# Kernel optimization log

Hardware: AMD Instinct MI355X
Metric: run time of the kernel (lower is better)

## Reference

```python
import jax, jax.numpy as jnp
import numpy as np

BATCH = 512          # bs_large + bs_small
COMBINED_BS = 320    # bs_large + bs_small // (r_large // r_small)
R = 64               # r_large
K = 4096             # hidden dim, fixed in the TIR kernel
N_ADAPT = 80         # combined adapters


def setup_inputs() -> dict:
    key = jax.random.key(0)
    k1, k2, k3, k4 = jax.random.split(key, 4)
    x = jax.random.normal(k1, (BATCH, 1, K), dtype=jnp.float32)
    xids = jax.random.randint(k2, (COMBINED_BS * R,), 0, BATCH, dtype=jnp.int32)
    wids = jax.random.randint(k3, (COMBINED_BS,), 0, N_ADAPT, dtype=jnp.int32)
    A = jax.random.normal(k4, (N_ADAPT, K, R), dtype=jnp.float32) * 0.02
    return {"x": x, "xids": xids, "wids": wids, "A": A}


def reference(x, xids, wids, A):
    # out[c, 0, r] = sum_k x[xids[c*R + r], 0, k] * A[wids[c], k, r]
    C = wids.shape[0]
    r = A.shape[2]
    tok = xids.reshape(C, r)          # per-output-element token ids
    xg = x[tok, 0, :]                 # (C, R, K) gathered activations
    Ag = A[wids]                      # (C, K, R) gathered adapters
    out = jnp.einsum('crk,ckr->cr', xg, Ag)
    return out[:, None, :]            # (C, 1, R)
```

## Files before the change

kernel.cpp:

```cpp
#include <hip/hip_runtime.h>
#include <stdint.h>

namespace {
constexpr int BATCH  = 512;
constexpr int CBS    = 320;
constexpr int R      = 64;
constexpr int K      = 4096;
constexpr int NADAPT = 80;
constexpr int SPLIT  = 8;
constexpr int KS     = K / SPLIT;
constexpr int TK     = 64;
constexpr int NT     = 256;
constexpr int NW     = NT / 64;
constexpr int NTILES = KS / TK;

constexpr size_t WS_X_OFF  = 4096;
constexpr size_t WS_NEEDED = WS_X_OFF + (size_t)BATCH * K * 2;

__device__ inline uint16_t f2bf(float f) {
    uint32_t u = __float_as_uint(f);
    u += 0x7fffu + ((u >> 16) & 1u);
    return (uint16_t)(u >> 16);
}
__device__ inline float bf2f(uint16_t b) {
    return __uint_as_float((uint32_t)b << 16);
}
__device__ inline float bflo(uint32_t u) { return __uint_as_float(u << 16); }
__device__ inline float bfhi(uint32_t u) { return __uint_as_float(u & 0xffff0000u); }
}

__global__ __launch_bounds__(256)
void prep(const float* __restrict__ x, uint16_t* __restrict__ xb,
          const int* __restrict__ wids, int* __restrict__ perm,
          float* __restrict__ out, int out_size)
{
    const int bid = blockIdx.x;
    const int t   = threadIdx.x;
    if (bid == 0) {
        __shared__ int hist[NADAPT];
        __shared__ int offs[NADAPT];
        if (t < NADAPT) hist[t] = 0;
        __syncthreads();
        for (int c = t; c < CBS; c += 256) atomicAdd(&hist[wids[c]], 1);
        __syncthreads();
        if (t == 0) {
            int run = 0;
            for (int i = 0; i < NADAPT; ++i) { offs[i] = run; run += hist[i]; }
        }
        __syncthreads();
        for (int c = t; c < CBS; c += 256) {
            const int pos = atomicAdd(&offs[wids[c]], 1);
            perm[pos] = c;
        }
    } else if (bid <= BATCH * K / 1024) {
        const int i = (bid - 1) * 256 + t;
        const float4 v = ((const float4*)x)[i];
        ushort4 o;
        o.x = f2bf(v.x); o.y = f2bf(v.y); o.z = f2bf(v.z); o.w = f2bf(v.w);
        ((ushort4*)xb)[i] = o;
    } else {
        const int i4 = (bid - (1 + BATCH * K / 1024)) * 256 + t;
        const int e  = i4 * 4;
        if (e + 3 < out_size) {
            ((float4*)out)[i4] = make_float4(0.f, 0.f, 0.f, 0.f);
        } else {
            for (int q = e; q < out_size; ++q) out[q] = 0.f;
        }
    }
}

__global__ __launch_bounds__(NT, 8)
void lora_main(const int* __restrict__ xids,
               const int* __restrict__ wids,
               const float* __restrict__ A,
               const uint16_t* __restrict__ xb,
               const int* __restrict__ perm,
               float* __restrict__ out)
{
    __shared__ uint32_t xs[2][(TK / 2) * R];
    __shared__ float red[NW * R];

    const int bid  = blockIdx.x;
    const int i0   = bid >> 3;
    const int s    = bid & 7;
    const int c    = perm[i0];
    const int t    = threadIdx.x;
    const int wv   = t >> 6;
    const int lane = t & 63;
    const int r4   = lane & 15;
    const int kq   = lane >> 4;

    const int wid = wids[c];
    const float* __restrict__ Aw = A + (size_t)wid * (K * R);

    const int kc = t & 15;
    const int rg = t >> 4;
    uint32_t rowoff[4];
#pragma unroll
    for (int j = 0; j < 4; ++j)
        rowoff[j] = (uint32_t)xids[c * R + 4 * rg + j] * K;
    const uint16_t* __restrict__ xbase = xb + (size_t)s * KS + kc * 4;
    const int colw = (4 * rg) ^ (kc << 2);
    const int w0i  = (2 * kc + 0) * R + colw;
    const int w1i  = (2 * kc + 1) * R + colw;

    const size_t aBase = (size_t)(s * KS + 16 * wv + 2 * kq) * R + 4 * r4;

    float4 acc = make_float4(0.f, 0.f, 0.f, 0.f);

    {
        uint2 L0 = *(const uint2*)(xbase + rowoff[0]);
        uint2 L1 = *(const uint2*)(xbase + rowoff[1]);
        uint2 L2 = *(const uint2*)(xbase + rowoff[2]);
        uint2 L3 = *(const uint2*)(xbase + rowoff[3]);
        *(uint4*)&xs[0][w0i] = make_uint4(L0.x, L1.x, L2.x, L3.x);
        *(uint4*)&xs[0][w1i] = make_uint4(L0.y, L1.y, L2.y, L3.y);
    }

    uint2 P0, P1, P2, P3;
    for (int tile = 0; tile < NTILES; ++tile) {
        const int nt = tile + 1;
        if (nt < NTILES) {
            const uint16_t* src = xbase + nt * TK;
            P0 = *(const uint2*)(src + rowoff[0]);
            P1 = *(const uint2*)(src + rowoff[1]);
            P2 = *(const uint2*)(src + rowoff[2]);
            P3 = *(const uint2*)(src + rowoff[3]);
        }
        __syncthreads();

        {
            const uint32_t* __restrict__ B = xs[tile & 1];
            const float* __restrict__ At = Aw + aBase + (size_t)tile * TK * R;
#pragma unroll
            for (int i = 0; i < 2; ++i) {
                const int k2  = wv * 8 + kq + 4 * i;
                const int col = (4 * r4) ^ (((k2 >> 1) & 15) << 2);
                const uint4 xv = *(const uint4*)&B[k2 * R + col];
                const float* Ap = At + (size_t)(8 * i) * R;
                const float4 a0 = *(const float4*)Ap;
                const float4 a1 = *(const float4*)(Ap + R);
                acc.x = fmaf(bflo(xv.x), a0.x, acc.x);
                acc.x = fmaf(bfhi(xv.x), a1.x, acc.x);
                acc.y = fmaf(bflo(xv.y), a0.y, acc.y);
                acc.y = fmaf(bfhi(xv.y), a1.y, acc.y);
                acc.z = fmaf(bflo(xv.z), a0.z, acc.z);
                acc.z = fmaf(bfhi(xv.z), a1.z, acc.z);
                acc.w = fmaf(bflo(xv.w), a0.w, acc.w);
                acc.w = fmaf(bfhi(xv.w), a1.w, acc.w);
            }
        }

        if (nt < NTILES) {
            const int b = nt & 1;
            *(uint4*)&xs[b][w0i] = make_uint4(P0.x, P1.x, P2.x, P3.x);
            *(uint4*)&xs[b][w1i] = make_uint4(P0.y, P1.y, P2.y, P3.y);
        }
    }

#pragma unroll
    for (int m = 16; m < 64; m <<= 1) {
        acc.x += __shfl_xor(acc.x, m, 64);
        acc.y += __shfl_xor(acc.y, m, 64);
        acc.z += __shfl_xor(acc.z, m, 64);
        acc.w += __shfl_xor(acc.w, m, 64);
    }
    __syncthreads();
    if (kq == 0) {
        float* rd = &red[wv * R + 4 * r4];
        rd[0] = acc.x; rd[1] = acc.y; rd[2] = acc.z; rd[3] = acc.w;
    }
    __syncthreads();
    if (wv == 0) {
        float sum = red[lane] + red[R + lane] + red[2 * R + lane] + red[3 * R + lane];
        atomicAdd(&out[c * R + lane], sum);
    }
}

__global__ __launch_bounds__(NT)
void lora_fallback(const float* __restrict__ x,
                   const int*   __restrict__ xids,
                   const int*   __restrict__ wids,
                   const float* __restrict__ A,
                   float*       __restrict__ out)
{
    __shared__ float xsf[TK * R];
    __shared__ float red[NW * R];
    const int bid  = blockIdx.x;
    const int c    = bid >> 3;
    const int s    = bid & 7;
    const int t    = threadIdx.x;
    const int wave = t >> 6;
    const int lane = t & 63;
    const int r4   = lane & 15;
    const int kq   = lane >> 4;
    const int wid  = wids[c];
    const float* __restrict__ Aw = A + (size_t)wid * (K * R);
    const int rw  = t >> 2;
    const int jq  = t & 3;
    const int tok = xids[c * R + rw];
    const float* __restrict__ xrow = x + (size_t)tok * K + s * KS + jq * 16;
    float4 acc = make_float4(0.f, 0.f, 0.f, 0.f);
    float4 pv[4];
    {
        const float4* src = (const float4*)xrow;
#pragma unroll
        for (int ii = 0; ii < 4; ++ii) pv[ii] = src[ii];
    }
    for (int tile = 0; tile < NTILES; ++tile) {
#pragma unroll
        for (int ii = 0; ii < 4; ++ii) {
            const int kk = jq * 16 + ii * 4;
            xsf[(kk + 0) * R + rw] = pv[ii].x;
            xsf[(kk + 1) * R + rw] = pv[ii].y;
            xsf[(kk + 2) * R + rw] = pv[ii].z;
            xsf[(kk + 3) * R + rw] = pv[ii].w;
        }
        __syncthreads();
        if (tile + 1 < NTILES) {
            const float4* src = (const float4*)(xrow + (tile + 1) * TK);
#pragma unroll
            for (int ii = 0; ii < 4; ++ii) pv[ii] = src[ii];
        }
        const int kw = wave * 16 + kq;
        const float* __restrict__ Ap =
            Aw + (size_t)(s * KS + tile * TK + kw) * R + 4 * r4;
#pragma unroll
        for (int i = 0; i < 4; ++i) {
            float4 av = *(const float4*)(Ap + (size_t)(4 * i) * R);
            float4 xv = *(const float4*)(&xsf[(kw + 4 * i) * R + 4 * r4]);
            acc.x = fmaf(xv.x, av.x, acc.x);
            acc.y = fmaf(xv.y, av.y, acc.y);
            acc.z = fmaf(xv.z, av.z, acc.z);
            acc.w = fmaf(xv.w, av.w, acc.w);
        }
        __syncthreads();
    }
#pragma unroll
    for (int m = 16; m < 64; m <<= 1) {
        acc.x += __shfl_xor(acc.x, m, 64);
        acc.y += __shfl_xor(acc.y, m, 64);
        acc.z += __shfl_xor(acc.z, m, 64);
        acc.w += __shfl_xor(acc.w, m, 64);
    }
    if (kq == 0) {
        float* rd = &red[wave * R + 4 * r4];
        rd[0] = acc.x; rd[1] = acc.y; rd[2] = acc.z; rd[3] = acc.w;
    }
    __syncthreads();
    if (wave == 0) {
        float sum = red[lane] + red[R + lane] + red[2 * R + lane] + red[3 * R + lane];
        atomicAdd(&out[c * R + lane], sum);
    }
}

extern "C" void kernel_launch(void* const* d_in, const int* in_sizes, int n_in,
                              void* d_out, int out_size, void* d_ws, size_t ws_size,
                              hipStream_t stream)
{
    (void)in_sizes; (void)n_in;
    const float* x    = (const float*)d_in[0];
    const int*   xids = (const int*)d_in[1];
    const int*   wids = (const int*)d_in[2];
    const float* A    = (const float*)d_in[3];
    float* out        = (float*)d_out;

    if (ws_size >= WS_NEEDED) {
        int*      perm = (int*)d_ws;
        uint16_t* xbw  = (uint16_t*)((char*)d_ws + WS_X_OFF);
        const int ncvt = BATCH * K / 1024;
        const int nz   = (out_size + 1023) / 1024;
        hipLaunchKernelGGL(prep, dim3(1 + ncvt + nz), dim3(256), 0, stream,
                           x, xbw, wids, perm, out, out_size);
        hipLaunchKernelGGL(lora_main, dim3(CBS * SPLIT), dim3(NT), 0, stream,
                           xids, wids, A, xbw, perm, out);
    } else {
        hipMemsetAsync(out, 0, (size_t)out_size * sizeof(float), stream);
        hipLaunchKernelGGL(lora_fallback, dim3(CBS * SPLIT), dim3(NT), 0, stream,
                           x, xids, wids, A, out);
    }
}
```

Baseline: 149.2 us.

## Process four combined rows per block with direct register loads, sharing A when adapters match

The main kernel is restructured. Each block now handles a group of four perm-sorted combined rows over one of 16 K-splits. Each thread owns one output column r and streams its gathered bf16 x row directly with 16-byte loads, dropping the LDS transpose, the double buffering and the block reductions. When the group's first and last rows share an adapter (sorted by perm), A values are loaded once and reused across all four rows, cutting A traffic. The trade-off is uncoalesced-looking per-thread x row loads (each lane reads a different token row) and more atomics per output.

```diff
diff --git a/kernel.cpp b/kernel.cpp
--- a/kernel.cpp
+++ b/kernel.cpp
@@ -7,12 +7,12 @@
 constexpr int R      = 64;
 constexpr int K      = 4096;
 constexpr int NADAPT = 80;
-constexpr int SPLIT  = 8;
+constexpr int GRP    = 4;
+constexpr int NGRP   = CBS / GRP;
+constexpr int SPLIT  = 16;
 constexpr int KS     = K / SPLIT;
-constexpr int TK     = 64;
+constexpr int KW     = KS / 4;
 constexpr int NT     = 256;
-constexpr int NW     = NT / 64;
-constexpr int NTILES = KS / TK;
 
 constexpr size_t WS_X_OFF  = 4096;
 constexpr size_t WS_NEEDED = WS_X_OFF + (size_t)BATCH * K * 2;
@@ -21,9 +21,6 @@
     uint32_t u = __float_as_uint(f);
     u += 0x7fffu + ((u >> 16) & 1u);
     return (uint16_t)(u >> 16);
-}
-__device__ inline float bf2f(uint16_t b) {
-    return __uint_as_float((uint32_t)b << 16);
 }
 __device__ inline float bflo(uint32_t u) { return __uint_as_float(u << 16); }
 __device__ inline float bfhi(uint32_t u) { return __uint_as_float(u & 0xffff0000u); }
@@ -69,7 +66,7 @@
     }
 }
 
-__global__ __launch_bounds__(NT, 8)
+__global__ __launch_bounds__(NT)
 void lora_main(const int* __restrict__ xids,
                const int* __restrict__ wids,
                const float* __restrict__ A,
@@ -77,104 +74,82 @@
                const int* __restrict__ perm,
                float* __restrict__ out)
 {
-    __shared__ uint32_t xs[2][(TK / 2) * R];
-    __shared__ float red[NW * R];
-
-    const int bid  = blockIdx.x;
-    const int i0   = bid >> 3;
-    const int s    = bid & 7;
-    const int c    = perm[i0];
-    const int t    = threadIdx.x;
-    const int wv   = t >> 6;
-    const int lane = t & 63;
-    const int r4   = lane & 15;
-    const int kq   = lane >> 4;
-
-    const int wid = wids[c];
-    const float* __restrict__ Aw = A + (size_t)wid * (K * R);
-
-    const int kc = t & 15;
-    const int rg = t >> 4;
-    uint32_t rowoff[4];
-#pragma unroll
-    for (int j = 0; j < 4; ++j)
-        rowoff[j] = (uint32_t)xids[c * R + 4 * rg + j] * K;
-    const uint16_t* __restrict__ xbase = xb + (size_t)s * KS + kc * 4;
-    const int colw = (4 * rg) ^ (kc << 2);
-    const int w0i  = (2 * kc + 0) * R + colw;
-    const int w1i  = (2 * kc + 1) * R + colw;
-
-    const size_t aBase = (size_t)(s * KS + 16 * wv + 2 * kq) * R + 4 * r4;
-
-    float4 acc = make_float4(0.f, 0.f, 0.f, 0.f);
-
-    {
-        uint2 L0 = *(const uint2*)(xbase + rowoff[0]);
-        uint2 L1 = *(const uint2*)(xbase + rowoff[1]);
-        uint2 L2 = *(const uint2*)(xbase + rowoff[2]);
-        uint2 L3 = *(const uint2*)(xbase + rowoff[3]);
-        *(uint4*)&xs[0][w0i] = make_uint4(L0.x, L1.x, L2.x, L3.x);
-        *(uint4*)&xs[0][w1i] = make_uint4(L0.y, L1.y, L2.y, L3.y);
-    }
-
-    uint2 P0, P1, P2, P3;
-    for (int tile = 0; tile < NTILES; ++tile) {
-        const int nt = tile + 1;
-        if (nt < NTILES) {
-            const uint16_t* src = xbase + nt * TK;
-            P0 = *(const uint2*)(src + rowoff[0]);
-            P1 = *(const uint2*)(src + rowoff[1]);
-            P2 = *(const uint2*)(src + rowoff[2]);
-            P3 = *(const uint2*)(src + rowoff[3]);
-        }
-        __syncthreads();
-
-        {
-            const uint32_t* __restrict__ B = xs[tile & 1];
-            const float* __restrict__ At = Aw + aBase + (size_t)tile * TK * R;
-#pragma unroll
-            for (int i = 0; i < 2; ++i) {
-                const int k2  = wv * 8 + kq + 4 * i;
-                const int col = (4 * r4) ^ (((k2 >> 1) & 15) << 2);
-                const uint4 xv = *(const uint4*)&B[k2 * R + col];
-                const float* Ap = At + (size_t)(8 * i) * R;
-                const float4 a0 = *(const float4*)Ap;
-                const float4 a1 = *(const float4*)(Ap + R);
-                acc.x = fmaf(bflo(xv.x), a0.x, acc.x);
-                acc.x = fmaf(bfhi(xv.x), a1.x, acc.x);
-                acc.y = fmaf(bflo(xv.y), a0.y, acc.y);
-                acc.y = fmaf(bfhi(xv.y), a1.y, acc.y);
-                acc.z = fmaf(bflo(xv.z), a0.z, acc.z);
-                acc.z = fmaf(bfhi(xv.z), a1.z, acc.z);
-                acc.w = fmaf(bflo(xv.w), a0.w, acc.w);
-                acc.w = fmaf(bfhi(xv.w), a1.w, acc.w);
+    const int bid = blockIdx.x;
+    const int g   = bid >> 4;
+    const int s   = bid & 15;
+    const int t   = threadIdx.x;
+    const int wv  = t >> 6;
+    const int r   = t & 63;
+    const int k0  = s * KS + wv * KW;
+
+    const int c0 = perm[GRP * g + 0], c1 = perm[GRP * g + 1],
+              c2 = perm[GRP * g + 2], c3 = perm[GRP * g + 3];
+    const int w0 = wids[c0], w1 = wids[c1], w2 = wids[c2], w3 = wids[c3];
+
+    const uint16_t* __restrict__ xp0 = xb + (size_t)xids[c0 * R + r] * K + k0;
+    const uint16_t* __restrict__ xp1 = xb + (size_t)xids[c1 * R + r] * K + k0;
+    const uint16_t* __restrict__ xp2 = xb + (size_t)xids[c2 * R + r] * K + k0;
+    const uint16_t* __restrict__ xp3 = xb + (size_t)xids[c3 * R + r] * K + k0;
+
+    const size_t kb = (size_t)k0 * R + r;
+    const float* __restrict__ A0 = A + (size_t)w0 * (K * R) + kb;
+    const float* __restrict__ A1 = A + (size_t)w1 * (K * R) + kb;
+    const float* __restrict__ A2 = A + (size_t)w2 * (K * R) + kb;
+    const float* __restrict__ A3 = A + (size_t)w3 * (K * R) + kb;
+
+    float acc0 = 0.f, acc1 = 0.f, acc2 = 0.f, acc3 = 0.f;
+
+#define FMA8(ACC, V, AP) do {                                              \
+        ACC = fmaf(bflo((V).x), (AP)[0], ACC);                             \
+        ACC = fmaf(bfhi((V).x), (AP)[1], ACC);                             \
+        ACC = fmaf(bflo((V).y), (AP)[2], ACC);                             \
+        ACC = fmaf(bfhi((V).y), (AP)[3], ACC);                             \
+        ACC = fmaf(bflo((V).z), (AP)[4], ACC);                             \
+        ACC = fmaf(bfhi((V).z), (AP)[5], ACC);                             \
+        ACC = fmaf(bflo((V).w), (AP)[6], ACC);                             \
+        ACC = fmaf(bfhi((V).w), (AP)[7], ACC);                             \
+    } while (0)
+
+    if (w0 == w3) {
+#pragma unroll 2
+        for (int kk = 0; kk < KW; kk += 8) {
+            const uint4 v0 = *(const uint4*)(xp0 + kk);
+            const uint4 v1 = *(const uint4*)(xp1 + kk);
+            const uint4 v2 = *(const uint4*)(xp2 + kk);
+            const uint4 v3 = *(const uint4*)(xp3 + kk);
+            float a[8];
+#pragma unroll
+            for (int q = 0; q < 8; ++q) a[q] = A0[(size_t)(kk + q) * R];
+            FMA8(acc0, v0, a);
+            FMA8(acc1, v1, a);
+            FMA8(acc2, v2, a);
+            FMA8(acc3, v3, a);
+        }
+    } else {
+#pragma unroll 2
+        for (int kk = 0; kk < KW; kk += 8) {
+            const uint4 v0 = *(const uint4*)(xp0 + kk);
+            const uint4 v1 = *(const uint4*)(xp1 + kk);
+            const uint4 v2 = *(const uint4*)(xp2 + kk);
+            const uint4 v3 = *(const uint4*)(xp3 + kk);
+            float a0[8], a1[8], a2[8], a3[8];
+#pragma unroll
+            for (int q = 0; q < 8; ++q) {
+                const size_t o = (size_t)(kk + q) * R;
+                a0[q] = A0[o]; a1[q] = A1[o]; a2[q] = A2[o]; a3[q] = A3[o];
             }
-        }
-
-        if (nt < NTILES) {
-            const int b = nt & 1;
-            *(uint4*)&xs[b][w0i] = make_uint4(P0.x, P1.x, P2.x, P3.x);
-            *(uint4*)&xs[b][w1i] = make_uint4(P0.y, P1.y, P2.y, P3.y);
-        }
-    }
-
-#pragma unroll
-    for (int m = 16; m < 64; m <<= 1) {
-        acc.x += __shfl_xor(acc.x, m, 64);
-        acc.y += __shfl_xor(acc.y, m, 64);
-        acc.z += __shfl_xor(acc.z, m, 64);
-        acc.w += __shfl_xor(acc.w, m, 64);
-    }
-    __syncthreads();
-    if (kq == 0) {
-        float* rd = &red[wv * R + 4 * r4];
-        rd[0] = acc.x; rd[1] = acc.y; rd[2] = acc.z; rd[3] = acc.w;
-    }
-    __syncthreads();
-    if (wv == 0) {
-        float sum = red[lane] + red[R + lane] + red[2 * R + lane] + red[3 * R + lane];
-        atomicAdd(&out[c * R + lane], sum);
-    }
+            FMA8(acc0, v0, a0);
+            FMA8(acc1, v1, a1);
+            FMA8(acc2, v2, a2);
+            FMA8(acc3, v3, a3);
+        }
+    }
+#undef FMA8
+
+    atomicAdd(&out[c0 * R + r], acc0);
+    atomicAdd(&out[c1 * R + r], acc1);
+    atomicAdd(&out[c2 * R + r], acc2);
+    atomicAdd(&out[c3 * R + r], acc3);
 }
 
 __global__ __launch_bounds__(NT)
@@ -184,8 +159,9 @@
                    const float* __restrict__ A,
                    float*       __restrict__ out)
 {
-    __shared__ float xsf[TK * R];
-    __shared__ float red[NW * R];
+    constexpr int FKS = 512, FTK = 64, FNT_TILES = 8, FNW = 4;
+    __shared__ float xsf[FTK * R];
+    __shared__ float red[FNW * R];
     const int bid  = blockIdx.x;
     const int c    = bid >> 3;
     const int s    = bid & 7;
@@ -199,7 +175,7 @@
     const int rw  = t >> 2;
     const int jq  = t & 3;
     const int tok = xids[c * R + rw];
-    const float* __restrict__ xrow = x + (size_t)tok * K + s * KS + jq * 16;
+    const float* __restrict__ xrow = x + (size_t)tok * K + s * FKS + jq * 16;
     float4 acc = make_float4(0.f, 0.f, 0.f, 0.f);
     float4 pv[4];
     {
@@ -207,7 +183,7 @@
 #pragma unroll
         for (int ii = 0; ii < 4; ++ii) pv[ii] = src[ii];
     }
-    for (int tile = 0; tile < NTILES; ++tile) {
+    for (int tile = 0; tile < FNT_TILES; ++tile) {
 #pragma unroll
         for (int ii = 0; ii < 4; ++ii) {
             const int kk = jq * 16 + ii * 4;
@@ -217,14 +193,14 @@
             xsf[(kk + 3) * R + rw] = pv[ii].w;
         }
         __syncthreads();
-        if (tile + 1 < NTILES) {
-            const float4* src = (const float4*)(xrow + (tile + 1) * TK);
+        if (tile + 1 < FNT_TILES) {
+            const float4* src = (const float4*)(xrow + (tile + 1) * FTK);
 #pragma unroll
             for (int ii = 0; ii < 4; ++ii) pv[ii] = src[ii];
         }
         const int kw = wave * 16 + kq;
         const float* __restrict__ Ap =
-            Aw + (size_t)(s * KS + tile * TK + kw) * R + 4 * r4;
+            Aw + (size_t)(s * FKS + tile * FTK + kw) * R + 4 * r4;
 #pragma unroll
         for (int i = 0; i < 4; ++i) {
             float4 av = *(const float4*)(Ap + (size_t)(4 * i) * R);
@@ -272,11 +248,11 @@
         const int nz   = (out_size + 1023) / 1024;
         hipLaunchKernelGGL(prep, dim3(1 + ncvt + nz), dim3(256), 0, stream,
                            x, xbw, wids, perm, out, out_size);
-        hipLaunchKernelGGL(lora_main, dim3(CBS * SPLIT), dim3(NT), 0, stream,
+        hipLaunchKernelGGL(lora_main, dim3(NGRP * SPLIT), dim3(NT), 0, stream,
                            xids, wids, A, xbw, perm, out);
     } else {
         hipMemsetAsync(out, 0, (size_t)out_size * sizeof(float), stream);
-        hipLaunchKernelGGL(lora_fallback, dim3(CBS * SPLIT), dim3(NT), 0, stream,
+        hipLaunchKernelGGL(lora_fallback, dim3(CBS * 8), dim3(NT), 0, stream,
                            x, xids, wids, A, out);
     }
 }
```

Result: slower. 179.9 us (+20.6%).
